# Optimization experiments

Measured on AMD Instinct MI355X. Metric: run time of the kernel, lower is better.

## Reference

```python
import jax, jax.numpy as jnp
import numpy as np

N0, N1, N2 = 1228800, 81920, 8192  # src nodes layer0, dst layer0 (=src layer1), dst layer1
D_IN, D_H, D_OUT = 128, 256, 64


def setup_inputs() -> dict:
    key = jax.random.key(0)
    ks = jax.random.split(key, 12)
    x = jax.random.normal(ks[0], (N0, D_IN), dtype=jnp.float32)
    src0 = jax.random.randint(ks[1], (N0,), 0, N0, dtype=jnp.int32)
    dst0 = jax.random.randint(ks[2], (N0,), 0, N1, dtype=jnp.int32)
    src1 = jax.random.randint(ks[3], (N1,), 0, N1, dtype=jnp.int32)
    dst1 = jax.random.randint(ks[4], (N1,), 0, N2, dtype=jnp.int32)
    s = lambda k, shape: jax.random.normal(k, shape, dtype=jnp.float32) * (1.0 / np.sqrt(shape[0]))
    return {
        "x": x, "src0": src0, "dst0": dst0, "src1": src1, "dst1": dst1,
        "Wself0": s(ks[5], (D_IN, D_H)), "Wneigh0": s(ks[6], (D_IN, D_H)),
        "b0": jnp.zeros((D_H,), jnp.float32),
        "Wself1": s(ks[7], (D_H, D_OUT)), "Wneigh1": s(ks[8], (D_H, D_OUT)),
        "b1": jnp.zeros((D_OUT,), jnp.float32),
    }


def _sage_mean(h_src, src, dst, num_dst, Wself, Wneigh, b):
    # gather messages from src, mean-reduce per dst (0 for isolated dst, like DGL)
    msg = h_src[src]  # [E, d]
    agg = jax.ops.segment_sum(msg, dst, num_segments=num_dst)
    deg = jax.ops.segment_sum(jnp.ones_like(dst, dtype=h_src.dtype), dst, num_segments=num_dst)
    h_neigh = agg / jnp.maximum(deg, 1.0)[:, None]
    h_dst = h_src[:num_dst]
    return h_dst @ Wself + h_neigh @ Wneigh + b


def reference(x, src0, dst0, src1, dst1, Wself0, Wneigh0, b0, Wself1, Wneigh1, b1):
    h = _sage_mean(x, src0, dst0, N1, Wself0, Wneigh0, b0)
    h = jax.nn.relu(h)  # Dropout(0.0) is identity
    h = _sage_mean(h, src1, dst1, N2, Wself1, Wneigh1, b1)
    return h
```

## Files before the change

### kernel.cpp

```cpp
#include <hip/hip_runtime.h>

#define N0c 1228800
#define N1c 81920
#define N2c 8192
#define D_IN 128
#define D_H 256
#define D_OUT 64
#define CAP 64

#define EDGE_BLKS (N0c / 256)
#define WPREP_BLKS 384

typedef __attribute__((ext_vector_type(8))) short short8;
typedef __attribute__((ext_vector_type(4))) float f32x4;

__device__ __forceinline__ unsigned f2b(float f) {
    unsigned u = __float_as_uint(f);
    return (u + 0x7FFFu + ((u >> 16) & 1u)) >> 16;
}
__device__ __forceinline__ float b2f(ushort s) {
    return __uint_as_float((unsigned)s << 16);
}

__global__ void k_fillprep(const int* __restrict__ src0, const int* __restrict__ dst0,
                           const int* __restrict__ src1, const int* __restrict__ dst1,
                           int* __restrict__ cnt0, int* __restrict__ cnt1,
                           int* __restrict__ srcs0, int* __restrict__ srcs1,
                           const float* __restrict__ Ws0, const float* __restrict__ Wn0,
                           const float* __restrict__ Ws1, const float* __restrict__ Wn1,
                           ushort* __restrict__ Wt0, ushort* __restrict__ Wt1)
{
    const int bid = blockIdx.x;
    if (bid < EDGE_BLKS) {
        const int i = bid * 256 + threadIdx.x;
        const int d = dst0[i];
        const int p = atomicAdd(&cnt0[d], 1);
        if (p < CAP) srcs0[d * CAP + p] = src0[i];
        if (i < N1c) {
            const int d1 = dst1[i];
            const int p1 = atomicAdd(&cnt1[d1], 1);
            if (p1 < CAP) srcs1[d1 * CAP + p1] = src1[i];
        }
    } else {
        int idx = (bid - EDGE_BLKS) * 256 + threadIdx.x;
        if (idx < 256 * 256) {
            const int n = idx >> 8, k = idx & 255;
            Wt0[n * 256 + k] = (ushort)f2b(k < 128 ? Ws0[k * 256 + n] : Wn0[(k - 128) * 256 + n]);
        } else {
            idx -= 256 * 256;
            const int n = idx >> 9, k = idx & 511;
            Wt1[n * 512 + k] = (ushort)f2b(k < 256 ? Ws1[k * 64 + n] : Wn1[(k - 256) * 64 + n]);
        }
    }
}

__global__ __launch_bounds__(256) void k_gather0w(
    const float* __restrict__ x, const int* __restrict__ cnt,
    const int* __restrict__ srcs, ushort* __restrict__ hnb)
{
    const int wid  = (blockIdx.x * 256 + threadIdx.x) >> 6;
    const int lane = threadIdx.x & 63;
    const int half = lane >> 5;
    const int li   = lane & 31;
    const int deg  = cnt[wid];
    const int dlim = deg < CAP ? deg : CAP;
    const int* sp  = srcs + (size_t)wid * CAP;
    const float4* x4 = reinterpret_cast<const float4*>(x);
    float ax = 0.f, ay = 0.f, az = 0.f, aw = 0.f;
    int j = 0;
    for (; j + 8 <= dlim; j += 8) {
        const int4 ia = *reinterpret_cast<const int4*>(sp + j);
        const int4 ib = *reinterpret_cast<const int4*>(sp + j + 4);
        const int s0 = half ? ia.y : ia.x;
        const int s1 = half ? ia.w : ia.z;
        const int s2 = half ? ib.y : ib.x;
        const int s3 = half ? ib.w : ib.z;
        const float4 v0 = x4[(size_t)s0 * 32 + li];
        const float4 v1 = x4[(size_t)s1 * 32 + li];
        const float4 v2 = x4[(size_t)s2 * 32 + li];
        const float4 v3 = x4[(size_t)s3 * 32 + li];
        ax += v0.x + v1.x + v2.x + v3.x;
        ay += v0.y + v1.y + v2.y + v3.y;
        az += v0.z + v1.z + v2.z + v3.z;
        aw += v0.w + v1.w + v2.w + v3.w;
    }
    for (; j + 2 <= dlim; j += 2) {
        const int2 ip = *reinterpret_cast<const int2*>(sp + j);
        const int s = half ? ip.y : ip.x;
        const float4 v = x4[(size_t)s * 32 + li];
        ax += v.x; ay += v.y; az += v.z; aw += v.w;
    }
    if (j < dlim) {
        const float4 v = x4[(size_t)sp[j] * 32 + li];
        if (!half) { ax += v.x; ay += v.y; az += v.z; aw += v.w; }
    }
    ax += __shfl_xor(ax, 32);
    ay += __shfl_xor(ay, 32);
    az += __shfl_xor(az, 32);
    aw += __shfl_xor(aw, 32);
    if (!half) {
        const float inv = 1.0f / fmaxf((float)deg, 1.0f);
        uint2 o;
        o.x = f2b(ax * inv) | (f2b(ay * inv) << 16);
        o.y = f2b(az * inv) | (f2b(aw * inv) << 16);
        reinterpret_cast<uint2*>(hnb + (size_t)wid * D_IN)[li] = o;
    }
}

__global__ __launch_bounds__(256) void k_mm0(
    const float* __restrict__ x, const ushort* __restrict__ hnb,
    const ushort* __restrict__ Wt, const float* __restrict__ bias,
    ushort* __restrict__ h)
{
    const int lane = threadIdx.x & 63;
    const int w    = threadIdx.x >> 6;
    const int lr   = lane & 15;
    const int lk   = (lane >> 4) << 3;
    const int mh   = w >> 1;
    const int ch   = w & 1;
    const int row0 = blockIdx.x * 64 + mh * 32 + lr;
    const int row1 = row0 + 16;

    short8 a0[8], a1[8];
#pragma unroll
    for (int s = 0; s < 4; ++s) {
        const float* p0 = x + (size_t)row0 * D_IN + s * 32 + lk;
        const float* p1 = x + (size_t)row1 * D_IN + s * 32 + lk;
        const float4 u0 = *reinterpret_cast<const float4*>(p0);
        const float4 v0 = *reinterpret_cast<const float4*>(p0 + 4);
        const float4 u1 = *reinterpret_cast<const float4*>(p1);
        const float4 v1 = *reinterpret_cast<const float4*>(p1 + 4);
        short8 t0, t1;
        t0[0]=(short)f2b(u0.x); t0[1]=(short)f2b(u0.y); t0[2]=(short)f2b(u0.z); t0[3]=(short)f2b(u0.w);
        t0[4]=(short)f2b(v0.x); t0[5]=(short)f2b(v0.y); t0[6]=(short)f2b(v0.z); t0[7]=(short)f2b(v0.w);
        t1[0]=(short)f2b(u1.x); t1[1]=(short)f2b(u1.y); t1[2]=(short)f2b(u1.z); t1[3]=(short)f2b(u1.w);
        t1[4]=(short)f2b(v1.x); t1[5]=(short)f2b(v1.y); t1[6]=(short)f2b(v1.z); t1[7]=(short)f2b(v1.w);
        a0[s] = t0; a1[s] = t1;
    }
#pragma unroll
    for (int c = 0; c < 4; ++c) {
        a0[4 + c] = *reinterpret_cast<const short8*>(hnb + (size_t)row0 * D_IN + c * 32 + lk);
        a1[4 + c] = *reinterpret_cast<const short8*>(hnb + (size_t)row1 * D_IN + c * 32 + lk);
    }

    f32x4 acc0[8], acc1[8];
#pragma unroll
    for (int nt = 0; nt < 8; ++nt) {
        acc0[nt] = (f32x4){0.f, 0.f, 0.f, 0.f};
        acc1[nt] = (f32x4){0.f, 0.f, 0.f, 0.f};
    }
#pragma unroll
    for (int nt = 0; nt < 8; ++nt) {
        const ushort* wp = Wt + (size_t)(ch * 128 + nt * 16 + lr) * 256 + lk;
#pragma unroll
        for (int s = 0; s < 8; ++s) {
            const short8 bf = *reinterpret_cast<const short8*>(wp + s * 32);
            acc0[nt] = __builtin_amdgcn_mfma_f32_16x16x32_bf16(a0[s], bf, acc0[nt], 0, 0, 0);
            acc1[nt] = __builtin_amdgcn_mfma_f32_16x16x32_bf16(a1[s], bf, acc1[nt], 0, 0, 0);
        }
    }

    const int rb0 = blockIdx.x * 64 + mh * 32 + ((lane >> 4) << 2);
    const int rb1 = rb0 + 16;
#pragma unroll
    for (int nt = 0; nt < 8; ++nt) {
        const int col = ch * 128 + nt * 16 + lr;
        const float bb = bias[col];
#pragma unroll
        for (int qq = 0; qq < 4; ++qq) {
            h[(size_t)(rb0 + qq) * D_H + col] = (ushort)f2b(fmaxf(acc0[nt][qq] + bb, 0.f));
            h[(size_t)(rb1 + qq) * D_H + col] = (ushort)f2b(fmaxf(acc1[nt][qq] + bb, 0.f));
        }
    }
}

__global__ __launch_bounds__(256) void k_mm1f(
    const ushort* __restrict__ h, const int* __restrict__ cnt,
    const int* __restrict__ srcs, const ushort* __restrict__ Wt,
    const float* __restrict__ bias, float* __restrict__ out)
{
    const int lane = threadIdx.x & 63;
    const int w    = threadIdx.x >> 6;
    const int lr   = lane & 15;
    const int lk   = (lane >> 4) << 3;
    const int grow = blockIdx.x * 64 + w * 16 + lr;

    short8 a[16];
#pragma unroll
    for (int s = 0; s < 8; ++s)
        a[s] = *reinterpret_cast<const short8*>(h + (size_t)grow * D_H + s * 32 + lk);

    float g[8][8];
#pragma unroll
    for (int c = 0; c < 8; ++c)
#pragma unroll
        for (int e = 0; e < 8; ++e) g[c][e] = 0.f;
    const int deg  = cnt[grow];
    const int dlim = deg < CAP ? deg : CAP;
    const int* sp  = srcs + (size_t)grow * CAP;
    for (int j = 0; j < dlim; ++j) {
        const int s0 = sp[j];
        const ushort* hp = h + (size_t)s0 * D_H + lk;
        short8 v[8];
#pragma unroll
        for (int c = 0; c < 8; ++c)
            v[c] = *reinterpret_cast<const short8*>(hp + c * 32);
#pragma unroll
        for (int c = 0; c < 8; ++c)
#pragma unroll
            for (int e = 0; e < 8; ++e) g[c][e] += b2f((ushort)v[c][e]);
    }
    const float inv = 1.0f / fmaxf((float)deg, 1.0f);
#pragma unroll
    for (int c = 0; c < 8; ++c) {
        short8 t;
#pragma unroll
        for (int e = 0; e < 8; ++e) t[e] = (short)f2b(g[c][e] * inv);
        a[8 + c] = t;
    }

    f32x4 acc[4];
#pragma unroll
    for (int nt = 0; nt < 4; ++nt) acc[nt] = (f32x4){0.f, 0.f, 0.f, 0.f};
#pragma unroll
    for (int nt = 0; nt < 4; ++nt) {
        const ushort* wp = Wt + (size_t)(nt * 16 + lr) * 512 + lk;
#pragma unroll
        for (int s = 0; s < 16; ++s) {
            const short8 bf = *reinterpret_cast<const short8*>(wp + s * 32);
            acc[nt] = __builtin_amdgcn_mfma_f32_16x16x32_bf16(a[s], bf, acc[nt], 0, 0, 0);
        }
    }

    const int rbase = blockIdx.x * 64 + w * 16 + ((lane >> 4) << 2);
#pragma unroll
    for (int nt = 0; nt < 4; ++nt) {
        const int col = nt * 16 + lr;
        const float bb = bias[col];
#pragma unroll
        for (int qq = 0; qq < 4; ++qq)
            out[(size_t)(rbase + qq) * D_OUT + col] = acc[nt][qq] + bb;
    }
}

extern "C" void kernel_launch(void* const* d_in, const int* in_sizes, int n_in,
                              void* d_out, int out_size, void* d_ws, size_t ws_size,
                              hipStream_t stream)
{
    const float* x      = (const float*)d_in[0];
    const int*   src0   = (const int*)d_in[1];
    const int*   dst0   = (const int*)d_in[2];
    const int*   src1   = (const int*)d_in[3];
    const int*   dst1   = (const int*)d_in[4];
    const float* Wself0 = (const float*)d_in[5];
    const float* Wneigh0= (const float*)d_in[6];
    const float* b0     = (const float*)d_in[7];
    const float* Wself1 = (const float*)d_in[8];
    const float* Wneigh1= (const float*)d_in[9];
    const float* b1     = (const float*)d_in[10];
    float* out = (float*)d_out;

    char* ws = (char*)d_ws;
    size_t woff = 0;
    auto take = [&](size_t bytes) -> void* {
        void* p = ws + woff;
        woff = (woff + bytes + 255) & ~(size_t)255;
        return p;
    };
    int*    cnt   = (int*)take((size_t)(N1c + N2c) * sizeof(int));
    int*    cnt0  = cnt;
    int*    cnt1  = cnt + N1c;
    int*    srcs0 = (int*)take((size_t)N1c * CAP * sizeof(int));
    int*    srcs1 = (int*)take((size_t)N2c * CAP * sizeof(int));
    ushort* Wt0   = (ushort*)take((size_t)256 * 256 * sizeof(ushort));
    ushort* Wt1   = (ushort*)take((size_t)64 * 512 * sizeof(ushort));
    ushort* h     = (ushort*)take((size_t)N1c * D_H * sizeof(ushort));
    ushort* hnb   = (ushort*)take((size_t)N1c * D_IN * sizeof(ushort));
    (void)ws_size;

    hipMemsetAsync(cnt, 0, (size_t)(N1c + N2c) * sizeof(int), stream);
    k_fillprep<<<EDGE_BLKS + WPREP_BLKS, 256, 0, stream>>>(
        src0, dst0, src1, dst1, cnt0, cnt1, srcs0, srcs1,
        Wself0, Wneigh0, Wself1, Wneigh1, Wt0, Wt1);
    k_gather0w<<<N1c / 4, 256, 0, stream>>>(x, cnt0, srcs0, hnb);
    k_mm0<<<N1c / 64, 256, 0, stream>>>(x, hnb, Wt0, b0, h);
    k_mm1f<<<N2c / 64, 256, 0, stream>>>(h, cnt1, srcs1, Wt1, b1, out);
}
```

Measured before the change: 298.1 us.

## Pre-convert x to bf16 and gather neighbor features from the bf16 copy

Adds a conversion pass inside the prep kernel that writes a bf16 copy of the whole input feature matrix. The neighbor gather and the first matmul then read this half-size copy instead of fp32, halving gather bytes and removing the per-tile conversion in the matmul. The cost is a full streaming read of x plus a write of the bf16 copy, and neighbor sums now use bf16-rounded inputs.

```diff
diff --git a/kernel.cpp b/kernel.cpp
--- a/kernel.cpp
+++ b/kernel.cpp
@@ -10,6 +10,7 @@
 
 #define EDGE_BLKS (N0c / 256)
 #define WPREP_BLKS 384
+#define CONV_BLKS 8192
 
 typedef __attribute__((ext_vector_type(8))) short short8;
 typedef __attribute__((ext_vector_type(4))) float f32x4;
@@ -22,13 +23,14 @@
     return __uint_as_float((unsigned)s << 16);
 }
 
-__global__ void k_fillprep(const int* __restrict__ src0, const int* __restrict__ dst0,
-                           const int* __restrict__ src1, const int* __restrict__ dst1,
-                           int* __restrict__ cnt0, int* __restrict__ cnt1,
-                           int* __restrict__ srcs0, int* __restrict__ srcs1,
-                           const float* __restrict__ Ws0, const float* __restrict__ Wn0,
-                           const float* __restrict__ Ws1, const float* __restrict__ Wn1,
-                           ushort* __restrict__ Wt0, ushort* __restrict__ Wt1)
+__global__ void k_prep(const int* __restrict__ src0, const int* __restrict__ dst0,
+                       const int* __restrict__ src1, const int* __restrict__ dst1,
+                       int* __restrict__ cnt0, int* __restrict__ cnt1,
+                       int* __restrict__ srcs0, int* __restrict__ srcs1,
+                       const float* __restrict__ Ws0, const float* __restrict__ Wn0,
+                       const float* __restrict__ Ws1, const float* __restrict__ Wn1,
+                       ushort* __restrict__ Wt0, ushort* __restrict__ Wt1,
+                       const float* __restrict__ x, ushort* __restrict__ xb)
 {
     const int bid = blockIdx.x;
     if (bid < EDGE_BLKS) {
@@ -41,7 +43,7 @@
             const int p1 = atomicAdd(&cnt1[d1], 1);
             if (p1 < CAP) srcs1[d1 * CAP + p1] = src1[i];
         }
-    } else {
+    } else if (bid < EDGE_BLKS + WPREP_BLKS) {
         int idx = (bid - EDGE_BLKS) * 256 + threadIdx.x;
         if (idx < 256 * 256) {
             const int n = idx >> 8, k = idx & 255;
@@ -51,64 +53,86 @@
             const int n = idx >> 9, k = idx & 511;
             Wt1[n * 512 + k] = (ushort)f2b(k < 256 ? Ws1[k * 64 + n] : Wn1[(k - 256) * 64 + n]);
         }
-    }
-}
-
-__global__ __launch_bounds__(256) void k_gather0w(
-    const float* __restrict__ x, const int* __restrict__ cnt,
+    } else {
+        const size_t total8 = (size_t)N0c * D_IN / 8;
+        const int cb = bid - EDGE_BLKS - WPREP_BLKS;
+        const f32x4* xv = reinterpret_cast<const f32x4*>(x);
+        short8* xo = reinterpret_cast<short8*>(xb);
+        for (size_t u = (size_t)cb * 256 + threadIdx.x; u < total8;
+             u += (size_t)CONV_BLKS * 256) {
+            const f32x4 a = __builtin_nontemporal_load(&xv[u * 2]);
+            const f32x4 b = __builtin_nontemporal_load(&xv[u * 2 + 1]);
+            short8 t;
+            t[0]=(short)f2b(a.x); t[1]=(short)f2b(a.y); t[2]=(short)f2b(a.z); t[3]=(short)f2b(a.w);
+            t[4]=(short)f2b(b.x); t[5]=(short)f2b(b.y); t[6]=(short)f2b(b.z); t[7]=(short)f2b(b.w);
+            xo[u] = t;
+        }
+    }
+}
+
+__global__ __launch_bounds__(256) void k_gather0b(
+    const ushort* __restrict__ xb, const int* __restrict__ cnt,
     const int* __restrict__ srcs, ushort* __restrict__ hnb)
 {
     const int wid  = (blockIdx.x * 256 + threadIdx.x) >> 6;
     const int lane = threadIdx.x & 63;
-    const int half = lane >> 5;
-    const int li   = lane & 31;
+    const int q    = lane >> 4;
+    const int li   = lane & 15;
     const int deg  = cnt[wid];
     const int dlim = deg < CAP ? deg : CAP;
     const int* sp  = srcs + (size_t)wid * CAP;
-    const float4* x4 = reinterpret_cast<const float4*>(x);
-    float ax = 0.f, ay = 0.f, az = 0.f, aw = 0.f;
+    const uint4* xv = reinterpret_cast<const uint4*>(xb);
+    float g[8];
+#pragma unroll
+    for (int e = 0; e < 8; ++e) g[e] = 0.f;
+
     int j = 0;
     for (; j + 8 <= dlim; j += 8) {
-        const int4 ia = *reinterpret_cast<const int4*>(sp + j);
-        const int4 ib = *reinterpret_cast<const int4*>(sp + j + 4);
-        const int s0 = half ? ia.y : ia.x;
-        const int s1 = half ? ia.w : ia.z;
-        const int s2 = half ? ib.y : ib.x;
-        const int s3 = half ? ib.w : ib.z;
-        const float4 v0 = x4[(size_t)s0 * 32 + li];
-        const float4 v1 = x4[(size_t)s1 * 32 + li];
-        const float4 v2 = x4[(size_t)s2 * 32 + li];
-        const float4 v3 = x4[(size_t)s3 * 32 + li];
-        ax += v0.x + v1.x + v2.x + v3.x;
-        ay += v0.y + v1.y + v2.y + v3.y;
-        az += v0.z + v1.z + v2.z + v3.z;
-        aw += v0.w + v1.w + v2.w + v3.w;
-    }
-    for (; j + 2 <= dlim; j += 2) {
-        const int2 ip = *reinterpret_cast<const int2*>(sp + j);
-        const int s = half ? ip.y : ip.x;
-        const float4 v = x4[(size_t)s * 32 + li];
-        ax += v.x; ay += v.y; az += v.z; aw += v.w;
-    }
-    if (j < dlim) {
-        const float4 v = x4[(size_t)sp[j] * 32 + li];
-        if (!half) { ax += v.x; ay += v.y; az += v.z; aw += v.w; }
-    }
-    ax += __shfl_xor(ax, 32);
-    ay += __shfl_xor(ay, 32);
-    az += __shfl_xor(az, 32);
-    aw += __shfl_xor(aw, 32);
-    if (!half) {
+        const int sa = sp[j + q];
+        const int sb = sp[j + 4 + q];
+        const uint4 va = xv[(size_t)sa * 16 + li];
+        const uint4 vb = xv[(size_t)sb * 16 + li];
+        g[0] += b2f((ushort)(va.x & 0xffff)) + b2f((ushort)(vb.x & 0xffff));
+        g[1] += b2f((ushort)(va.x >> 16))    + b2f((ushort)(vb.x >> 16));
+        g[2] += b2f((ushort)(va.y & 0xffff)) + b2f((ushort)(vb.y & 0xffff));
+        g[3] += b2f((ushort)(va.y >> 16))    + b2f((ushort)(vb.y >> 16));
+        g[4] += b2f((ushort)(va.z & 0xffff)) + b2f((ushort)(vb.z & 0xffff));
+        g[5] += b2f((ushort)(va.z >> 16))    + b2f((ushort)(vb.z >> 16));
+        g[6] += b2f((ushort)(va.w & 0xffff)) + b2f((ushort)(vb.w & 0xffff));
+        g[7] += b2f((ushort)(va.w >> 16))    + b2f((ushort)(vb.w >> 16));
+    }
+    for (; j < dlim; j += 4) {
+        if (j + q < dlim) {
+            const int s = sp[j + q];
+            const uint4 v = xv[(size_t)s * 16 + li];
+            g[0] += b2f((ushort)(v.x & 0xffff));
+            g[1] += b2f((ushort)(v.x >> 16));
+            g[2] += b2f((ushort)(v.y & 0xffff));
+            g[3] += b2f((ushort)(v.y >> 16));
+            g[4] += b2f((ushort)(v.z & 0xffff));
+            g[5] += b2f((ushort)(v.z >> 16));
+            g[6] += b2f((ushort)(v.w & 0xffff));
+            g[7] += b2f((ushort)(v.w >> 16));
+        }
+    }
+#pragma unroll
+    for (int e = 0; e < 8; ++e) {
+        g[e] += __shfl_xor(g[e], 16);
+        g[e] += __shfl_xor(g[e], 32);
+    }
+    if (lane < 16) {
         const float inv = 1.0f / fmaxf((float)deg, 1.0f);
-        uint2 o;
-        o.x = f2b(ax * inv) | (f2b(ay * inv) << 16);
-        o.y = f2b(az * inv) | (f2b(aw * inv) << 16);
-        reinterpret_cast<uint2*>(hnb + (size_t)wid * D_IN)[li] = o;
+        uint4 o;
+        o.x = f2b(g[0] * inv) | (f2b(g[1] * inv) << 16);
+        o.y = f2b(g[2] * inv) | (f2b(g[3] * inv) << 16);
+        o.z = f2b(g[4] * inv) | (f2b(g[5] * inv) << 16);
+        o.w = f2b(g[6] * inv) | (f2b(g[7] * inv) << 16);
+        reinterpret_cast<uint4*>(hnb + (size_t)wid * D_IN)[li] = o;
     }
 }
 
 __global__ __launch_bounds__(256) void k_mm0(
-    const float* __restrict__ x, const ushort* __restrict__ hnb,
+    const ushort* __restrict__ xb, const ushort* __restrict__ hnb,
     const ushort* __restrict__ Wt, const float* __restrict__ bias,
     ushort* __restrict__ h)
 {
@@ -124,18 +148,8 @@
     short8 a0[8], a1[8];
 #pragma unroll
     for (int s = 0; s < 4; ++s) {
-        const float* p0 = x + (size_t)row0 * D_IN + s * 32 + lk;
-        const float* p1 = x + (size_t)row1 * D_IN + s * 32 + lk;
-        const float4 u0 = *reinterpret_cast<const float4*>(p0);
-        const float4 v0 = *reinterpret_cast<const float4*>(p0 + 4);
-        const float4 u1 = *reinterpret_cast<const float4*>(p1);
-        const float4 v1 = *reinterpret_cast<const float4*>(p1 + 4);
-        short8 t0, t1;
-        t0[0]=(short)f2b(u0.x); t0[1]=(short)f2b(u0.y); t0[2]=(short)f2b(u0.z); t0[3]=(short)f2b(u0.w);
-        t0[4]=(short)f2b(v0.x); t0[5]=(short)f2b(v0.y); t0[6]=(short)f2b(v0.z); t0[7]=(short)f2b(v0.w);
-        t1[0]=(short)f2b(u1.x); t1[1]=(short)f2b(u1.y); t1[2]=(short)f2b(u1.z); t1[3]=(short)f2b(u1.w);
-        t1[4]=(short)f2b(v1.x); t1[5]=(short)f2b(v1.y); t1[6]=(short)f2b(v1.z); t1[7]=(short)f2b(v1.w);
-        a0[s] = t0; a1[s] = t1;
+        a0[s] = *reinterpret_cast<const short8*>(xb + (size_t)row0 * D_IN + s * 32 + lk);
+        a1[s] = *reinterpret_cast<const short8*>(xb + (size_t)row1 * D_IN + s * 32 + lk);
     }
 #pragma unroll
     for (int c = 0; c < 4; ++c) {
@@ -276,13 +290,14 @@
     ushort* Wt1   = (ushort*)take((size_t)64 * 512 * sizeof(ushort));
     ushort* h     = (ushort*)take((size_t)N1c * D_H * sizeof(ushort));
     ushort* hnb   = (ushort*)take((size_t)N1c * D_IN * sizeof(ushort));
+    ushort* xb    = (ushort*)take((size_t)N0c * D_IN * sizeof(ushort));
     (void)ws_size;
 
     hipMemsetAsync(cnt, 0, (size_t)(N1c + N2c) * sizeof(int), stream);
-    k_fillprep<<<EDGE_BLKS + WPREP_BLKS, 256, 0, stream>>>(
+    k_prep<<<EDGE_BLKS + WPREP_BLKS + CONV_BLKS, 256, 0, stream>>>(
         src0, dst0, src1, dst1, cnt0, cnt1, srcs0, srcs1,
-        Wself0, Wneigh0, Wself1, Wneigh1, Wt0, Wt1);
-    k_gather0w<<<N1c / 4, 256, 0, stream>>>(x, cnt0, srcs0, hnb);
-    k_mm0<<<N1c / 64, 256, 0, stream>>>(x, hnb, Wt0, b0, h);
+        Wself0, Wneigh0, Wself1, Wneigh1, Wt0, Wt1, x, xb);
+    k_gather0b<<<N1c / 4, 256, 0, stream>>>(xb, cnt0, srcs0, hnb);
+    k_mm0<<<N1c / 64, 256, 0, stream>>>(xb, hnb, Wt0, b0, h);
     k_mm1f<<<N2c / 64, 256, 0, stream>>>(h, cnt1, srcs1, Wt1, b1, out);
 }
```

After: 437.9 us. 46.9% more time.
